# Kernel optimization log

Measured on AMD Instinct MI355X. Metric: run time of the kernel, lower is better.

## Reference

```python
import jax, jax.numpy as jnp
import numpy as np

B, D, X, Y = 16, 64, 48, 48
DI = 128            # interactions_dim
DIN = D + 2         # depth_dim + 2 coord channels (qst_dim = 0)


def setup_inputs() -> dict:
    key = jax.random.key(0)
    k1, k2, k3, k4 = jax.random.split(key, 4)
    x = jax.random.normal(k1, (B, D, X, Y), dtype=jnp.float32)
    s = 1.0 / np.sqrt(DIN)  # torch Linear default init range
    Wq = jax.random.uniform(k2, (DI, DIN), jnp.float32, -s, s)
    Wk = jax.random.uniform(k3, (DI, DIN), jnp.float32, -s, s)
    Wv = jax.random.uniform(k4, (DI, DIN), jnp.float32, -s, s)
    return {"x": x, "Wq": Wq, "Wk": Wk, "Wv": Wv}


def _add_xy(x):
    # addXYfeatures: append normalized grid coords, flatten spatial dims
    b, d, sx, sy = x.shape
    fx = -1.0 + (jnp.arange(sx, dtype=x.dtype) + 0.5) * (2.0 / sx)
    fy = -1.0 + (jnp.arange(sy, dtype=x.dtype) + 0.5) * (2.0 / sy)
    fxy = jnp.broadcast_to(fx[None, None, :, None], (b, 1, sx, sy))
    fyx = jnp.broadcast_to(fy[None, None, None, :], (b, 1, sx, sy))
    aug = jnp.concatenate([x, fxy, fyx], axis=1)  # [B, D+2, X, Y]
    return aug.reshape(b, d + 2, sx * sy)          # [B, D+2, N]


def reference(x, Wq, Wk, Wv):
    aug = _add_xy(x)                               # [B, Din, N]
    e = jnp.transpose(aug, (0, 2, 1))              # [B, N, Din] entities
    q = jnp.einsum('bnd,ed->bne', e, Wq)           # [B, N, DI]
    k = jnp.einsum('bnd,ed->bne', e, Wk)
    v = jnp.einsum('bnd,ed->bne', e, Wv)
    scale = 1.0 / jnp.sqrt(jnp.asarray(DI, dtype=x.dtype))
    scores = jnp.einsum('bqe,bke->bqk', q, k) * scale  # [B, Nq, Nk]
    # torch: F.softmax(..., dim=0) on per-batch [Nq, Nk] -> axis=1 here (over queries)
    att = jax.nn.softmax(scores, axis=1)
    out = jnp.einsum('bqk,bkd->bqd', att, v)       # [B, N, DI]
    return out
```

## Files before the change

kernel.cpp:

```cpp
#include <hip/hip_runtime.h>
#include <cstdint>

#define B_    16
#define D_    64
#define N_    2304
#define DI_   128
#define S2_   0.12751875732488788f
#define NB_   ((size_t)B_ * N_ * DI_)
#define KTSZ_ 4096
#define VTSZ_ 5120
#define NKT_  72
#define NKH_  18
#define OF4_  1179648

typedef __attribute__((ext_vector_type(8)))  short short8v;
typedef __attribute__((ext_vector_type(16))) float f32x16;

#if defined(__has_builtin)
#if __has_builtin(__builtin_amdgcn_exp2f)
#define EXP2(x) __builtin_amdgcn_exp2f(x)
#else
#define EXP2(x) exp2f(x)
#endif
#else
#define EXP2(x) exp2f(x)
#endif

__device__ __forceinline__ unsigned short f2bf(float f) {
    unsigned u = __builtin_bit_cast(unsigned, f);
    u = (u + 0x7FFFu + ((u >> 16) & 1u)) >> 16;
    return (unsigned short)u;
}
__device__ __forceinline__ float bf2f(unsigned short h) {
    unsigned u = ((unsigned)h) << 16;
    return __builtin_bit_cast(float, u);
}
__device__ __forceinline__ unsigned cvtpk_bf16(float lo, float hi) {
    unsigned r;
    asm volatile("v_cvt_pk_bf16_f32 %0, %1, %2" : "=v"(r) : "v"(lo), "v"(hi));
    return r;
}
__device__ __forceinline__ void plswap(unsigned &a, unsigned &b) {
    asm volatile("v_permlane32_swap_b32 %0, %1" : "+v"(a), "+v"(b));
}

__device__ __forceinline__ void stage_k(const unsigned short* g,
                                        unsigned short* l_, int w, int ln) {
    #pragma unroll
    for (int i = 0; i < 2; ++i)
        __builtin_amdgcn_global_load_lds(
            (const __attribute__((address_space(1))) void*)(g + i * 2048 + w * 512 + ln * 8),
            (__attribute__((address_space(3))) void*)(l_ + i * 2048 + w * 512), 16, 0, 0);
}
__device__ __forceinline__ void stage_v(const unsigned short* g,
                                        unsigned short* l_, int w, int ln, int t) {
    #pragma unroll
    for (int i = 0; i < 2; ++i)
        __builtin_amdgcn_global_load_lds(
            (const __attribute__((address_space(1))) void*)(g + i * 2048 + w * 512 + ln * 8),
            (__attribute__((address_space(3))) void*)(l_ + i * 2048 + w * 512), 16, 0, 0);
    if (t < 128)
        __builtin_amdgcn_global_load_lds(
            (const __attribute__((address_space(1))) void*)(g + 4096 + w * 512 + ln * 8),
            (__attribute__((address_space(3))) void*)(l_ + 4096 + w * 512), 16, 0, 0);
}

__global__ __launch_bounds__(256) void prep_kernel(
    const float* __restrict__ Wq, const float* __restrict__ Wk,
    const float* __restrict__ Wv, unsigned short* __restrict__ W3p,
    float* __restrict__ Zg)
{
    const int t = threadIdx.x;
    if (blockIdx.x == 0) {
        for (int r = t; r < 384; r += 256) {
            const float* src = (r < 128) ? (Wq + r * 66)
                             : (r < 256) ? (Wk + (r - 128) * 66) : (Wv + (r - 256) * 66);
            for (int c = 0; c < 66; ++c) W3p[r * 88 + c] = f2bf(src[c]);
            for (int c = 66; c < 88; ++c) W3p[r * 88 + c] = 0;
        }
    } else {
        Zg[(blockIdx.x - 1) * 256 + t] = 0.0f;
    }
}

__global__ __launch_bounds__(256) void qkv_kernel(
    const float* __restrict__ x, const unsigned short* __restrict__ W3p,
    unsigned short* __restrict__ Qb, unsigned short* __restrict__ Ksw,
    unsigned short* __restrict__ Vn)
{
    __shared__ unsigned short Es[128 * 88];
    const int t = threadIdx.x;
    const int b = blockIdx.x / 18, nt = blockIdx.x - b * 18;
    const int n0 = nt * 128;

    {
        const int d = t & 63, q4 = t >> 6;
        const float* xp = x + ((size_t)b * D_ + d) * N_ + n0 + q4 * 32;
        float xv[32];
        #pragma unroll
        for (int i = 0; i < 8; ++i) *(float4*)(xv + 4 * i) = *(const float4*)(xp + 4 * i);
        #pragma unroll
        for (int i = 0; i < 32; ++i) Es[(q4 * 32 + i) * 88 + d] = f2bf(xv[i]);
    }
    if (t < 128) {
        int n = n0 + t;
        int ix = n / 48, iy = n - ix * 48;
        Es[t * 88 + 64] = f2bf(-1.0f + ((float)ix + 0.5f) * (2.0f / 48.0f));
        Es[t * 88 + 65] = f2bf(-1.0f + ((float)iy + 0.5f) * (2.0f / 48.0f));
        #pragma unroll
        for (int m = 0; m < 11; ++m) *(unsigned*)&Es[t * 88 + 66 + 2 * m] = 0;
    }
    __syncthreads();

    const int l = t & 63, w = t >> 6;
    const int m32 = l & 31, H = l >> 5;
    const int colbase = w * 96;
    #pragma unroll
    for (int nf = 0; nf < 4; ++nf) {
        f32x16 acc[3];
        #pragma unroll
        for (int of = 0; of < 3; ++of)
            #pragma unroll
            for (int i = 0; i < 16; ++i) acc[of][i] = 0.0f;
        #pragma unroll
        for (int kc = 0; kc < 5; ++kc) {
            short8v a = *(const short8v*)&Es[(nf * 32 + m32) * 88 + kc * 16 + H * 8];
            #pragma unroll
            for (int of = 0; of < 3; ++of) {
                short8v bf = *(const short8v*)&W3p[(colbase + of * 32 + m32) * 88 + kc * 16 + H * 8];
                acc[of] = __builtin_amdgcn_mfma_f32_32x32x16_bf16(a, bf, acc[of], 0, 0, 0);
            }
        }
        #pragma unroll
        for (int of = 0; of < 3; ++of) {
            const int col0 = colbase + of * 32;
            const int mi = col0 >> 7, e0 = col0 & 127;
            const int e = e0 + m32;
            if (mi == 0) {
                #pragma unroll
                for (int r = 0; r < 16; ++r) {
                    int n = n0 + nf * 32 + (r & 3) + 8 * (r >> 2) + 4 * H;
                    Qb[((size_t)b * N_ + n) * DI_ + e] = f2bf(acc[of][r] * S2_);
                }
            } else if (mi == 1) {
                const size_t tbase = ((size_t)b * NKT_ + nt * 4 + nf) * KTSZ_;
                const int cx = e >> 3, ei = e & 7;
                #pragma unroll
                for (int r = 0; r < 16; ++r) {
                    int rr = (r & 3) + 8 * (r >> 2) + 4 * H;
                    Ksw[tbase + rr * 128 + ((cx ^ (rr & 15)) * 8) + ei] = f2bf(acc[of][r]);
                }
            } else {
                #pragma unroll
                for (int r = 0; r < 16; ++r) {
                    int n = n0 + nf * 32 + (r & 3) + 8 * (r >> 2) + 4 * H;
                    Vn[((size_t)b * N_ + n) * DI_ + e] = f2bf(acc[of][r]);
                }
            }
        }
    }
}

__global__ __launch_bounds__(256, 4) void zsum_kernel(
    const unsigned short* __restrict__ Qb, const unsigned short* __restrict__ Ksw,
    float* __restrict__ Zg)
{
    __shared__ unsigned short Ks0[KTSZ_], Ks1[KTSZ_];
    __shared__ float Zacc[576];
    const int t = threadIdx.x;
    const int blk = blockIdx.x;
    const int b = 2 * (blk & 7) + ((blk >> 3) & 1);
    const int rest = blk >> 4;
    const int qt = rest % 18, kh = rest / 18;
    const int q0 = qt * 128;
    const int l = t & 63, w = t >> 6;
    const int m32 = l & 31, H = l >> 5;

    for (int i = t; i < 576; i += 256) Zacc[i] = 0.0f;

    short8v qreg[8];
    {
        const unsigned short* qp = Qb + ((size_t)b * N_ + q0 + w * 32 + m32) * DI_ + H * 8;
        #pragma unroll
        for (int ec = 0; ec < 8; ++ec) qreg[ec] = *(const short8v*)(qp + ec * 16);
    }
    int ka[8];
    #pragma unroll
    for (int ec = 0; ec < 8; ++ec)
        ka[ec] = m32 * 128 + (((ec * 2 + H) ^ (m32 & 15)) * 8);

    const unsigned short* kswb = Ksw + ((size_t)b * NKT_ + kh * NKH_) * KTSZ_;
    stage_k(kswb, Ks0, w, l);
    asm volatile("s_waitcnt vmcnt(0)" ::: "memory");
    __syncthreads();

#define ZSUM_STEP(KB, KTC)                                                     \
    {                                                                          \
        f32x16 sa, sb;                                                         \
        _Pragma("unroll") for (int i = 0; i < 16; ++i) { sa[i] = 0.f; sb[i] = 0.f; } \
        __builtin_amdgcn_s_setprio(1);                                         \
        _Pragma("unroll") for (int ec = 0; ec < 8; ++ec) {                     \
            short8v bk = *(const short8v*)&(KB)[ka[ec]];                       \
            if (ec & 1) sb = __builtin_amdgcn_mfma_f32_32x32x16_bf16(qreg[ec], bk, sb, 0, 0, 0); \
            else        sa = __builtin_amdgcn_mfma_f32_32x32x16_bf16(qreg[ec], bk, sa, 0, 0, 0); \
        }                                                                      \
        __builtin_amdgcn_s_setprio(0);                                         \
        float zl = 0.0f;                                                       \
        _Pragma("unroll") for (int r = 0; r < 16; ++r) zl += EXP2(sa[r] + sb[r]); \
        atomicAdd(&Zacc[(KTC) * 32 + m32], zl);                                \
        asm volatile("s_waitcnt vmcnt(0)" ::: "memory");                       \
        __syncthreads();                                                       \
    }

    for (int kt = 0; kt < NKH_; kt += 2) {
        stage_k(kswb + (size_t)(kt + 1) * KTSZ_, Ks1, w, l);
        ZSUM_STEP(Ks0, kt);
        if (kt + 2 < NKH_) stage_k(kswb + (size_t)(kt + 2) * KTSZ_, Ks0, w, l);
        ZSUM_STEP(Ks1, kt + 1);
    }
    for (int i = t; i < 576; i += 256)
        atomicAdd(&Zg[(size_t)b * N_ + kh * 576 + i], Zacc[i]);
}

__global__ __launch_bounds__(256) void repackV_kernel(
    const unsigned short* __restrict__ Vn, const float* __restrict__ Zg,
    unsigned short* __restrict__ Vsw)
{
    __shared__ unsigned short Vstg[32 * 132];
    __shared__ float zinv[32];
    const int blk = blockIdx.x;
    const int b = blk / NKT_, kt = blk - b * NKT_;
    const int t = threadIdx.x;
    const int k0 = kt * 32;
    {
        const int k = t >> 3, c = (t & 7) * 16;
        const unsigned short* src = Vn + ((size_t)b * N_ + k0 + k) * DI_ + c;
        *(int4*)&Vstg[k * 132 + c]     = *(const int4*)(src);
        *(int4*)&Vstg[k * 132 + c + 8] = *(const int4*)(src + 8);
    }
    if (t < 32) zinv[t] = 1.0f / Zg[(size_t)b * N_ + k0 + t];
    __syncthreads();
    unsigned short* dstt = Vsw + ((size_t)b * NKT_ + kt) * VTSZ_;
    const int d = t & 127, part = t >> 7;
    #pragma unroll
    for (int g = 0; g < 4; ++g) {
        unsigned short sv[4];
        #pragma unroll
        for (int j = 0; j < 4; ++j) {
            int k = part * 16 + g * 4 + j;
            sv[j] = f2bf(bf2f(Vstg[k * 132 + d]) * zinv[k]);
        }
        *(int2*)(dstt + d * 40 + part * 16 + g * 4) = *(const int2*)sv;
    }
}

__global__ __launch_bounds__(256, 3) void attn_kernel(
    const unsigned short* __restrict__ Qb, const unsigned short* __restrict__ Ksw,
    const unsigned short* __restrict__ Vsw,
    float* __restrict__ O0, float* __restrict__ Op)
{
    __shared__ unsigned short Ks0[KTSZ_], Ks1[KTSZ_];
    __shared__ unsigned short Vs0[VTSZ_], Vs1[VTSZ_];
    const int t = threadIdx.x;
    const int blk = blockIdx.x;
    const int b = 2 * (blk & 7) + ((blk >> 3) & 1);
    const int rest = blk >> 4;
    const int qt = rest % 18, kh = rest / 18;
    const int q0 = qt * 128;
    const int l = t & 63, w = t >> 6;
    const int m32 = l & 31, H = l >> 5;

    short8v qreg[8];
    {
        const unsigned short* qp = Qb + ((size_t)b * N_ + q0 + w * 32 + m32) * DI_ + H * 8;
        #pragma unroll
        for (int ec = 0; ec < 8; ++ec) qreg[ec] = *(const short8v*)(qp + ec * 16);
    }
    f32x16 oacc[4];
    #pragma unroll
    for (int df = 0; df < 4; ++df)
        #pragma unroll
        for (int i = 0; i < 16; ++i) oacc[df][i] = 0.0f;

    int ka[8];
    #pragma unroll
    for (int ec = 0; ec < 8; ++ec)
        ka[ec] = m32 * 128 + (((ec * 2 + H) ^ (m32 & 15)) * 8);
    const int vb0 = m32 * 40 + H * 8;

    const unsigned short* kswb = Ksw + ((size_t)b * NKT_ + kh * NKH_) * KTSZ_;
    const unsigned short* vswb = Vsw + ((size_t)b * NKT_ + kh * NKH_) * VTSZ_;
    stage_k(kswb, Ks0, w, l);
    stage_v(vswb, Vs0, w, l, t);
    asm volatile("s_waitcnt vmcnt(0)" ::: "memory");
    __syncthreads();

#define ATTN_STEP(KB, VB)                                                      \
    {                                                                          \
        f32x16 sa, sb;                                                         \
        _Pragma("unroll") for (int i = 0; i < 16; ++i) { sa[i] = 0.f; sb[i] = 0.f; } \
        __builtin_amdgcn_s_setprio(1);                                         \
        _Pragma("unroll") for (int ec = 0; ec < 8; ++ec) {                     \
            short8v ak = *(const short8v*)&(KB)[ka[ec]];                       \
            if (ec & 1) sb = __builtin_amdgcn_mfma_f32_32x32x16_bf16(ak, qreg[ec], sb, 0, 0, 0); \
            else        sa = __builtin_amdgcn_mfma_f32_32x32x16_bf16(ak, qreg[ec], sa, 0, 0, 0); \
        }                                                                      \
        __builtin_amdgcn_s_setprio(0);                                         \
        float p[16];                                                           \
        _Pragma("unroll") for (int r = 0; r < 16; ++r) p[r] = EXP2(sa[r] + sb[r]); \
        unsigned c0[4], c1[4];                                                 \
        _Pragma("unroll") for (int m = 0; m < 4; ++m) {                        \
            c0[m] = cvtpk_bf16(p[4 * m],     p[4 * m + 1]);                    \
            c1[m] = cvtpk_bf16(p[4 * m + 2], p[4 * m + 3]);                    \
        }                                                                      \
        short8v pB[2];                                                         \
        _Pragma("unroll") for (int kq = 0; kq < 2; ++kq) {                     \
            unsigned d0 = c0[2 * kq], d2 = c0[2 * kq + 1]; plswap(d0, d2);     \
            unsigned d1 = c1[2 * kq], d3 = c1[2 * kq + 1]; plswap(d1, d3);     \
            int4 t4; t4.x = (int)d0; t4.y = (int)d1; t4.z = (int)d2; t4.w = (int)d3; \
            pB[kq] = __builtin_bit_cast(short8v, t4);                          \
        }                                                                      \
        __builtin_amdgcn_s_setprio(1);                                         \
        _Pragma("unroll") for (int df = 0; df < 4; ++df) {                     \
            _Pragma("unroll") for (int kq = 0; kq < 2; ++kq) {                 \
                short8v av = *(const short8v*)&(VB)[vb0 + df * 1280 + kq * 16]; \
                oacc[df] = __builtin_amdgcn_mfma_f32_32x32x16_bf16(av, pB[kq], oacc[df], 0, 0, 0); \
            }                                                                  \
        }                                                                      \
        __builtin_amdgcn_s_setprio(0);                                         \
        asm volatile("s_waitcnt vmcnt(0)" ::: "memory");                       \
        __syncthreads();                                                       \
    }

    for (int kt = 0; kt < NKH_; kt += 2) {
        stage_k(kswb + (size_t)(kt + 1) * KTSZ_, Ks1, w, l);
        stage_v(vswb + (size_t)(kt + 1) * VTSZ_, Vs1, w, l, t);
        ATTN_STEP(Ks0, Vs0);
        if (kt + 2 < NKH_) {
            stage_k(kswb + (size_t)(kt + 2) * KTSZ_, Ks0, w, l);
            stage_v(vswb + (size_t)(kt + 2) * VTSZ_, Vs0, w, l, t);
        }
        ATTN_STEP(Ks1, Vs1);
    }

    float* outp = (kh == 0 ? O0 : (Op + (size_t)(kh - 1) * NB_))
                + ((size_t)b * N_ + q0 + w * 32 + m32) * DI_;
    #pragma unroll
    for (int df = 0; df < 4; ++df)
        #pragma unroll
        for (int r = 0; r < 16; ++r) {
            int d = df * 32 + (r & 3) + 8 * (r >> 2) + 4 * H;
            outp[d] = oacc[df][r];
        }
}

__global__ __launch_bounds__(256) void reduce_kernel(
    float* __restrict__ out, const float* __restrict__ part)
{
    const size_t idx = (size_t)blockIdx.x * 256 + threadIdx.x;
    float4 p0 = ((const float4*)part)[idx];
    float4 p1 = ((const float4*)part)[idx + (size_t)OF4_];
    float4 p2 = ((const float4*)part)[idx + 2 * (size_t)OF4_];
    float4 o  = ((float4*)out)[idx];
    o.x += p0.x + p1.x + p2.x;
    o.y += p0.y + p1.y + p2.y;
    o.z += p0.z + p1.z + p2.z;
    o.w += p0.w + p1.w + p2.w;
    ((float4*)out)[idx] = o;
}

extern "C" void kernel_launch(void* const* d_in, const int* in_sizes, int n_in,
                              void* d_out, int out_size, void* d_ws, size_t ws_size,
                              hipStream_t stream)
{
    const float* x  = (const float*)d_in[0];
    const float* Wq = (const float*)d_in[1];
    const float* Wk = (const float*)d_in[2];
    const float* Wv = (const float*)d_in[3];

    unsigned short* Qb  = (unsigned short*)d_ws;
    unsigned short* Ksw = Qb  + NB_;
    unsigned short* Vsw = Ksw + NB_;
    unsigned short* W3p = Vsw + (size_t)B_ * NKT_ * VTSZ_;
    float*          Zg  = (float*)(W3p + 384 * 88);
    float*          Op  = Zg + (size_t)B_ * N_;
    unsigned short* Vn  = (unsigned short*)Op;
    float* out = (float*)d_out;

    prep_kernel   <<<145,  256, 0, stream>>>(Wq, Wk, Wv, W3p, Zg);
    qkv_kernel    <<<288,  256, 0, stream>>>(x, W3p, Qb, Ksw, Vn);
    zsum_kernel   <<<1152, 256, 0, stream>>>(Qb, Ksw, Zg);
    repackV_kernel<<<1152, 256, 0, stream>>>(Vn, Zg, Vsw);
    attn_kernel   <<<1152, 256, 0, stream>>>(Qb, Ksw, Vsw, out, Op);
    reduce_kernel <<<4608, 256, 0, stream>>>(out, Op);
}
```

Baseline: 154.6 us.

## Double query tile per block in zsum and use a single accumulator chain in attn

The zsum kernel now processes 256 queries per block (two 32-row fragments per wave), so each staged K tile in shared memory is reused by twice as many MFMAs and the grid halves to 576 blocks. It also lowers the occupancy hint to make room for the extra query registers. In the attention kernel the two alternating score accumulators are merged into one dependent MFMA chain, with exp2 fused into the bf16 packing, which cuts registers but serializes the MFMAs. The risks are lower occupancy and wave count in zsum and longer MFMA dependency latency in attn.

```diff
diff --git a/kernel.cpp b/kernel.cpp
--- a/kernel.cpp
+++ b/kernel.cpp
@@ -161,7 +161,7 @@
     }
 }
 
-__global__ __launch_bounds__(256, 4) void zsum_kernel(
+__global__ __launch_bounds__(256, 3) void zsum_kernel(
     const unsigned short* __restrict__ Qb, const unsigned short* __restrict__ Ksw,
     float* __restrict__ Zg)
 {
@@ -171,18 +171,21 @@
     const int blk = blockIdx.x;
     const int b = 2 * (blk & 7) + ((blk >> 3) & 1);
     const int rest = blk >> 4;
-    const int qt = rest % 18, kh = rest / 18;
-    const int q0 = qt * 128;
+    const int qt = rest % 9, kh = rest / 9;
+    const int q0 = qt * 256;
     const int l = t & 63, w = t >> 6;
     const int m32 = l & 31, H = l >> 5;
 
     for (int i = t; i < 576; i += 256) Zacc[i] = 0.0f;
 
-    short8v qreg[8];
+    short8v qreg[2][8];
     {
-        const unsigned short* qp = Qb + ((size_t)b * N_ + q0 + w * 32 + m32) * DI_ + H * 8;
-        #pragma unroll
-        for (int ec = 0; ec < 8; ++ec) qreg[ec] = *(const short8v*)(qp + ec * 16);
+        const unsigned short* qp = Qb + ((size_t)b * N_ + q0 + w * 64 + m32) * DI_ + H * 8;
+        #pragma unroll
+        for (int qf = 0; qf < 2; ++qf)
+            #pragma unroll
+            for (int ec = 0; ec < 8; ++ec)
+                qreg[qf][ec] = *(const short8v*)(qp + (size_t)qf * 32 * DI_ + ec * 16);
     }
     int ka[8];
     #pragma unroll
@@ -194,30 +197,34 @@
     asm volatile("s_waitcnt vmcnt(0)" ::: "memory");
     __syncthreads();
 
-#define ZSUM_STEP(KB, KTC)                                                     \
+#define ZSTEP(KB, KTC)                                                         \
     {                                                                          \
-        f32x16 sa, sb;                                                         \
-        _Pragma("unroll") for (int i = 0; i < 16; ++i) { sa[i] = 0.f; sb[i] = 0.f; } \
+        f32x16 s0, s1;                                                         \
+        _Pragma("unroll") for (int i = 0; i < 16; ++i) { s0[i] = 0.f; s1[i] = 0.f; } \
         __builtin_amdgcn_s_setprio(1);                                         \
         _Pragma("unroll") for (int ec = 0; ec < 8; ++ec) {                     \
             short8v bk = *(const short8v*)&(KB)[ka[ec]];                       \
-            if (ec & 1) sb = __builtin_amdgcn_mfma_f32_32x32x16_bf16(qreg[ec], bk, sb, 0, 0, 0); \
-            else        sa = __builtin_amdgcn_mfma_f32_32x32x16_bf16(qreg[ec], bk, sa, 0, 0, 0); \
+            s0 = __builtin_amdgcn_mfma_f32_32x32x16_bf16(qreg[0][ec], bk, s0, 0, 0, 0); \
+            s1 = __builtin_amdgcn_mfma_f32_32x32x16_bf16(qreg[1][ec], bk, s1, 0, 0, 0); \
         }                                                                      \
         __builtin_amdgcn_s_setprio(0);                                         \
         float zl = 0.0f;                                                       \
-        _Pragma("unroll") for (int r = 0; r < 16; ++r) zl += EXP2(sa[r] + sb[r]); \
+        _Pragma("unroll") for (int r = 0; r < 16; ++r)                         \
+            zl += EXP2(s0[r]) + EXP2(s1[r]);                                   \
         atomicAdd(&Zacc[(KTC) * 32 + m32], zl);                                \
         asm volatile("s_waitcnt vmcnt(0)" ::: "memory");                       \
         __syncthreads();                                                       \
     }
 
-    for (int kt = 0; kt < NKH_; kt += 2) {
+    for (int g = 0; g < 9; ++g) {
+        const int kt = 2 * g;
         stage_k(kswb + (size_t)(kt + 1) * KTSZ_, Ks1, w, l);
-        ZSUM_STEP(Ks0, kt);
+        ZSTEP(Ks0, kt);
         if (kt + 2 < NKH_) stage_k(kswb + (size_t)(kt + 2) * KTSZ_, Ks0, w, l);
-        ZSUM_STEP(Ks1, kt + 1);
-    }
+        ZSTEP(Ks1, kt + 1);
+    }
+#undef ZSTEP
+
     for (int i = t; i < 576; i += 256)
         atomicAdd(&Zg[(size_t)b * N_ + kh * 576 + i], Zacc[i]);
 }
@@ -295,23 +302,22 @@
     asm volatile("s_waitcnt vmcnt(0)" ::: "memory");
     __syncthreads();
 
-#define ATTN_STEP(KB, VB)                                                      \
+#define PSTEP(KB, VB)                                                          \
     {                                                                          \
-        f32x16 sa, sb;                                                         \
-        _Pragma("unroll") for (int i = 0; i < 16; ++i) { sa[i] = 0.f; sb[i] = 0.f; } \
+        f32x16 sacc;                                                           \
+        _Pragma("unroll") for (int i = 0; i < 16; ++i) sacc[i] = 0.f;          \
         __builtin_amdgcn_s_setprio(1);                                         \
         _Pragma("unroll") for (int ec = 0; ec < 8; ++ec) {                     \
             short8v ak = *(const short8v*)&(KB)[ka[ec]];                       \
-            if (ec & 1) sb = __builtin_amdgcn_mfma_f32_32x32x16_bf16(ak, qreg[ec], sb, 0, 0, 0); \
-            else        sa = __builtin_amdgcn_mfma_f32_32x32x16_bf16(ak, qreg[ec], sa, 0, 0, 0); \
+            sacc = __builtin_amdgcn_mfma_f32_32x32x16_bf16(ak, qreg[ec], sacc, 0, 0, 0); \
         }                                                                      \
         __builtin_amdgcn_s_setprio(0);                                         \
-        float p[16];                                                           \
-        _Pragma("unroll") for (int r = 0; r < 16; ++r) p[r] = EXP2(sa[r] + sb[r]); \
         unsigned c0[4], c1[4];                                                 \
         _Pragma("unroll") for (int m = 0; m < 4; ++m) {                        \
-            c0[m] = cvtpk_bf16(p[4 * m],     p[4 * m + 1]);                    \
-            c1[m] = cvtpk_bf16(p[4 * m + 2], p[4 * m + 3]);                    \
+            float e0 = EXP2(sacc[4 * m]),     e1 = EXP2(sacc[4 * m + 1]);      \
+            float e2 = EXP2(sacc[4 * m + 2]), e3 = EXP2(sacc[4 * m + 3]);      \
+            c0[m] = cvtpk_bf16(e0, e1);                                        \
+            c1[m] = cvtpk_bf16(e2, e3);                                        \
         }                                                                      \
         short8v pB[2];                                                         \
         _Pragma("unroll") for (int kq = 0; kq < 2; ++kq) {                     \
@@ -335,13 +341,14 @@
     for (int kt = 0; kt < NKH_; kt += 2) {
         stage_k(kswb + (size_t)(kt + 1) * KTSZ_, Ks1, w, l);
         stage_v(vswb + (size_t)(kt + 1) * VTSZ_, Vs1, w, l, t);
-        ATTN_STEP(Ks0, Vs0);
+        PSTEP(Ks0, Vs0);
         if (kt + 2 < NKH_) {
             stage_k(kswb + (size_t)(kt + 2) * KTSZ_, Ks0, w, l);
             stage_v(vswb + (size_t)(kt + 2) * VTSZ_, Vs0, w, l, t);
         }
-        ATTN_STEP(Ks1, Vs1);
-    }
+        PSTEP(Ks1, Vs1);
+    }
+#undef PSTEP
 
     float* outp = (kh == 0 ? O0 : (Op + (size_t)(kh - 1) * NB_))
                 + ((size_t)b * N_ + q0 + w * 32 + m32) * DI_;
@@ -389,7 +396,7 @@
 
     prep_kernel   <<<145,  256, 0, stream>>>(Wq, Wk, Wv, W3p, Zg);
     qkv_kernel    <<<288,  256, 0, stream>>>(x, W3p, Qb, Ksw, Vn);
-    zsum_kernel   <<<1152, 256, 0, stream>>>(Qb, Ksw, Zg);
+    zsum_kernel   <<<576,  256, 0, stream>>>(Qb, Ksw, Zg);
     repackV_kernel<<<1152, 256, 0, stream>>>(Vn, Zg, Vsw);
     attn_kernel   <<<1152, 256, 0, stream>>>(Qb, Ksw, Vsw, out, Op);
     reduce_kernel <<<4608, 256, 0, stream>>>(out, Op);
```

Result: faster. 146.5 us (median of 2 runs) (-5.3%).
